# Optimization experiments

Hardware: AMD Instinct MI355X
Metric: run time of the kernel (lower is better)

Reference implementation:

```python
import jax, jax.numpy as jnp
import numpy as np

B, N, FIN, H, F = 8, 1024, 256, 8, 64
NEG_SLOPE = 0.2


def setup_inputs() -> dict:
    key = jax.random.key(0)
    k = jax.random.split(key, 6)
    x = jax.random.normal(k[0], (B, N, FIN), dtype=jnp.float32)
    adj_mask = jax.random.randint(k[1], (B, N, N), 0, 2, dtype=jnp.int32)
    edge_prior = jax.random.normal(k[2], (B, N, N), dtype=jnp.float32)
    # params (xavier-style scales)
    W = jax.random.normal(k[3], (FIN, H * F), dtype=jnp.float32) * np.sqrt(2.0 / (FIN + H * F))
    a_left = jax.random.normal(k[4], (H, F), dtype=jnp.float32) * np.sqrt(2.0 / (1 + F))
    a_right = jax.random.normal(k[5], (H, F), dtype=jnp.float32) * np.sqrt(2.0 / (1 + F))
    edge_scale = jnp.float32(0.05)
    return {"x": x, "adj_mask": adj_mask, "edge_prior": edge_prior,
            "W": W, "a_left": a_left, "a_right": a_right, "edge_scale": edge_scale}


def reference(x, adj_mask, edge_prior, W, a_left, a_right, edge_scale):
    b, n, _ = x.shape
    h = (x @ W).reshape(b, n, H, F)                      # [B,N,H,F]
    e_left = jnp.einsum('bnhf,hf->bnh', h, a_left)       # [B,N,H]
    e_right = jnp.einsum('bnhf,hf->bnh', h, a_right)     # [B,N,H]
    e = jax.nn.leaky_relu(e_left[:, :, None, :] + e_right[:, None, :, :],
                          negative_slope=NEG_SLOPE)      # [B,N,N,H]
    e = e + edge_scale * edge_prior[..., None]
    e = jnp.where((adj_mask == 0)[..., None], -jnp.inf, e)
    alpha = jax.nn.softmax(e, axis=2)                    # softmax over neighbors j
    h_new = jnp.einsum('bijh,bjhf->bihf', alpha, h)      # [B,N,H,F]
    return h_new.reshape(b, n, H * F)                    # concat=True
```

## Files before the change

kernel.cpp:

```cpp
#include <hip/hip_runtime.h>
#include <hip/hip_bf16.h>

#define B_ 8
#define N_ 1024
#define FIN_ 256
#define H_ 8
#define F_ 64
#define HF_ 512
#define BN_ 8192
#define LOG2E 1.4426950408889634f

using bf16x8 = __attribute__((ext_vector_type(8))) short;
using f32x4  = __attribute__((ext_vector_type(4))) float;
using i32x4  = __attribute__((ext_vector_type(4))) int;

__device__ __forceinline__ short f2bf(float x) {
  __hip_bfloat16 b = __float2bfloat16(x);
  return *reinterpret_cast<short*>(&b);
}
__device__ __forceinline__ float bf2f(short s) {
  union { unsigned u; float f; } v;
  v.u = ((unsigned)(unsigned short)s) << 16;
  return v.f;
}
__device__ __forceinline__ bf16x8 cvtCE(f32x4 pa, f32x4 pb, i32x4 ma, i32x4 mb, float es) {
  bf16x8 o;
#pragma unroll
  for (int e = 0; e < 4; e++) {
    o[e]     = f2bf(ma[e] != 0 ? es * pa[e] : -1e30f);
    o[e + 4] = f2bf(mb[e] != 0 ? es * pb[e] : -1e30f);
  }
  return o;
}

__global__ __launch_bounds__(256) void k_cvt(
    const float* __restrict__ x, const float* __restrict__ W,
    short* __restrict__ xb, short* __restrict__ Wt) {
  const int bid = blockIdx.x;
  if (bid < 1024) {
    const int idx = (bid * 256 + threadIdx.x) * 8;
    f32x4 a = *(const f32x4*)(x + idx);
    f32x4 b = *(const f32x4*)(x + idx + 4);
    bf16x8 o;
    o[0]=f2bf(a[0]); o[1]=f2bf(a[1]); o[2]=f2bf(a[2]); o[3]=f2bf(a[3]);
    o[4]=f2bf(b[0]); o[5]=f2bf(b[1]); o[6]=f2bf(b[2]); o[7]=f2bf(b[3]);
    *(bf16x8*)(xb + idx) = o;
  } else {
    const int idx = (bid - 1024) * 256 + threadIdx.x;
    const int f = idx >> 8, c = idx & 255;
    Wt[f * FIN_ + c] = f2bf(W[c * HF_ + f]);
  }
}

__global__ __launch_bounds__(256) void k_pre(
    const float* __restrict__ prior, const int* __restrict__ mask,
    const float* __restrict__ esp, short* __restrict__ cmat) {
  const int b  = blockIdx.x & 7;
  const int it = blockIdx.x >> 3;
  const int t  = threadIdx.x;
  const int i  = t >> 3;
  const int jb = (t & 7) * 8;
  const float es = esp[0] * LOG2E;
  const size_t rowbase = ((size_t)b * N_ + it * 32 + i) * N_;
  short* cmt = cmat + (size_t)(b * 32 + it) * 32768
             + (i >> 4) * 512 + (i & 15) * 8;
#pragma unroll
  for (int jt = 0; jt < 16; jt++) {
    const int j = jt * 64 + jb;
    f32x4 p0 = *(const f32x4*)(prior + rowbase + j);
    f32x4 p1 = *(const f32x4*)(prior + rowbase + j + 4);
    i32x4 m0 = *(const i32x4*)(mask + rowbase + j);
    i32x4 m1 = *(const i32x4*)(mask + rowbase + j + 4);
    *(bf16x8*)(cmt + (j >> 5) * 1024 + ((j >> 3) & 3) * 128) =
        cvtCE(p0, p1, m0, m1, es);
  }
}

__global__ __launch_bounds__(256) void k_h(
    const short* __restrict__ Wt, const short* __restrict__ xb,
    const float* __restrict__ aL, const float* __restrict__ aR,
    short* __restrict__ hAg, float* __restrict__ el_t, float* __restrict__ er_t) {
  const int nt = blockIdx.x;
  const int h  = blockIdx.y;
  const int w  = threadIdx.x >> 6;
  const int l  = threadIdx.x & 63;
  const int lr = l & 15, lk = l >> 4;
  const int n0 = nt * 64;
  const int fbase = h * 64 + w * 16;

  f32x4 acc[4] = {};
  const short* arow = Wt + (fbase + lr) * FIN_ + lk * 8;

#pragma unroll
  for (int k0 = 0; k0 < FIN_; k0 += 32) {
    bf16x8 a = *(const bf16x8*)(arow + k0);
#pragma unroll
    for (int nf = 0; nf < 4; nf++) {
      bf16x8 bb = *(const bf16x8*)(xb + (size_t)(n0 + nf * 16 + lr) * FIN_ + k0 + lk * 8);
      acc[nf] = __builtin_amdgcn_mfma_f32_16x16x32_bf16(a, bb, acc[nf], 0, 0, 0);
    }
  }

  __shared__ short sT[64][72];
  __shared__ float sEl[4][64], sEr[4][64];
  float al[4], ar[4];
#pragma unroll
  for (int r = 0; r < 4; r++) {
    const int fl = w * 16 + lk * 4 + r;
    al[r] = aL[h * F_ + fl];
    ar[r] = aR[h * F_ + fl];
  }
#pragma unroll
  for (int nf = 0; nf < 4; nf++) {
    const int nl = nf * 16 + lr;
#pragma unroll
    for (int r = 0; r < 4; r++)
      sT[w * 16 + lk * 4 + r][nl] = f2bf(acc[nf][r]);
    float pl = acc[nf][0]*al[0] + acc[nf][1]*al[1] + acc[nf][2]*al[2] + acc[nf][3]*al[3];
    float pr = acc[nf][0]*ar[0] + acc[nf][1]*ar[1] + acc[nf][2]*ar[2] + acc[nf][3]*ar[3];
    pl += __shfl_xor(pl, 16); pl += __shfl_xor(pl, 32);
    pr += __shfl_xor(pr, 16); pr += __shfl_xor(pr, 32);
    if (lk == 0) { sEl[w][nl] = pl; sEr[w][nl] = pr; }
  }
  __syncthreads();
  if (threadIdx.x < 64) {
    const int n = threadIdx.x;
    el_t[h * BN_ + n0 + n] = (sEl[0][n] + sEl[1][n] + sEl[2][n] + sEl[3][n]) * LOG2E;
    er_t[h * BN_ + n0 + n] = (sEr[0][n] + sEr[1][n] + sEr[2][n] + sEr[3][n]) * LOG2E;
  }
  const int b8h = (nt >> 4) * 8 + h;
  const int jb  = (nt & 15) * 2;
#pragma unroll
  for (int gi = 0; gi < 2; gi++) {
    const int g   = threadIdx.x * 2 + gi;
    const int jsl = g >> 8, ff = (g >> 6) & 3, gl = g & 63;
    const int glr = gl & 15, glk = gl >> 4;
    bf16x8 v = *(const bf16x8*)(&sT[ff * 16 + glr][jsl * 32 + glk * 8]);
    *(bf16x8*)(hAg + (((size_t)b8h * 32 + jb + jsl) * 4 + ff) * 512 + gl * 8) = v;
  }
}

#define PREFX(sn, Hd, E0d, E1d, Cd)                                   \
  {                                                                   \
    const short* hs_ = hW + (size_t)(sn) * 2048;                      \
    Hd[0] = *(const bf16x8*)(hs_);                                    \
    Hd[1] = *(const bf16x8*)(hs_ + 512);                              \
    Hd[2] = *(const bf16x8*)(hs_ + 1024);                             \
    Hd[3] = *(const bf16x8*)(hs_ + 1536);                             \
    E0d   = *(const f32x4*)(erp + (sn) * 32);                         \
    E1d   = *(const f32x4*)(erp + (sn) * 32 + 4);                     \
    Cd[0] = *(const bf16x8*)(cmW + (size_t)(sn) * 1024);              \
    Cd[1] = *(const bf16x8*)(cmW + (size_t)(sn) * 1024 + 512);        \
  }

#define COMP2(Hu, Cu, E0u, E1u)                                                \
  {                                                                            \
    bf16x8 pfA, pfB;                                                           \
    _Pragma("unroll")                                                          \
    for (int q = 0; q < 4; q++) {                                              \
      const float e0 = E0u[q], e1 = E1u[q];                                    \
      float sA  = el0 + e0, sA2 = el0 + e1;                                    \
      float sB  = el1 + e0, sB2 = el1 + e1;                                    \
      float vA  = fmaf(0.6f, sA,  bf2f(Cu[0][q]));                             \
      vA  = fmaf(0.4f, fabsf(sA),  vA);                                        \
      float vA2 = fmaf(0.6f, sA2, bf2f(Cu[0][q + 4]));                         \
      vA2 = fmaf(0.4f, fabsf(sA2), vA2);                                       \
      float vB  = fmaf(0.6f, sB,  bf2f(Cu[1][q]));                             \
      vB  = fmaf(0.4f, fabsf(sB),  vB);                                        \
      float vB2 = fmaf(0.6f, sB2, bf2f(Cu[1][q + 4]));                         \
      vB2 = fmaf(0.4f, fabsf(sB2), vB2);                                       \
      float x1_, x2_, x3_, x4_;                                                \
      asm("v_exp_f32 %0, %1" : "=v"(x1_) : "v"(vA));                           \
      asm("v_exp_f32 %0, %1" : "=v"(x2_) : "v"(vA2));                          \
      asm("v_exp_f32 %0, %1" : "=v"(x3_) : "v"(vB));                           \
      asm("v_exp_f32 %0, %1" : "=v"(x4_) : "v"(vB2));                          \
      pfA[q] = f2bf(x1_); pfA[q + 4] = f2bf(x2_);                              \
      pfB[q] = f2bf(x3_); pfB[q + 4] = f2bf(x4_);                              \
    }                                                                          \
    __builtin_amdgcn_s_setprio(1);                                             \
    accSA   = __builtin_amdgcn_mfma_f32_16x16x32_bf16(ones, pfA, accSA, 0,0,0);\
    accSB   = __builtin_amdgcn_mfma_f32_16x16x32_bf16(ones, pfB, accSB, 0,0,0);\
    accA[0] = __builtin_amdgcn_mfma_f32_16x16x32_bf16(Hu[0], pfA, accA[0],0,0,0);\
    accB[0] = __builtin_amdgcn_mfma_f32_16x16x32_bf16(Hu[0], pfB, accB[0],0,0,0);\
    accA[1] = __builtin_amdgcn_mfma_f32_16x16x32_bf16(Hu[1], pfA, accA[1],0,0,0);\
    accB[1] = __builtin_amdgcn_mfma_f32_16x16x32_bf16(Hu[1], pfB, accB[1],0,0,0);\
    accA[2] = __builtin_amdgcn_mfma_f32_16x16x32_bf16(Hu[2], pfA, accA[2],0,0,0);\
    accB[2] = __builtin_amdgcn_mfma_f32_16x16x32_bf16(Hu[2], pfB, accB[2],0,0,0);\
    accA[3] = __builtin_amdgcn_mfma_f32_16x16x32_bf16(Hu[3], pfA, accA[3],0,0,0);\
    accB[3] = __builtin_amdgcn_mfma_f32_16x16x32_bf16(Hu[3], pfB, accB[3],0,0,0);\
    __builtin_amdgcn_s_setprio(0);                                             \
  }

__global__ __launch_bounds__(256, 2) void k_attn(
    const short* __restrict__ hAg, const float* __restrict__ el_t,
    const float* __restrict__ er_t, const short* __restrict__ cmat,
    float* __restrict__ out) {
  const int bid = blockIdx.x;
  const int b  = bid & 7;
  const int hp = (bid >> 3) & 1;
  const int it = bid >> 4;
  const int t  = threadIdx.x;
  const int h  = hp * 4 + (t >> 6);
  const int l  = t & 63;
  const int lr = l & 15, lk = l >> 4;
  const int i0 = it * 32;
  const size_t bn = (size_t)b * N_;

  const float el0 = el_t[h * BN_ + bn + i0 + lr];
  const float el1 = el_t[h * BN_ + bn + i0 + 16 + lr];
  const float* erp = er_t + h * BN_ + bn + lk * 8;
  const short* hW  = hAg + (size_t)(b * 8 + h) * 65536 + l * 8;
  const short* cmW = cmat + (size_t)(b * 32 + it) * 32768 + l * 8;

  bf16x8 HA[4], HB[4], HC[4], HD[4];
  bf16x8 cA[2], cB[2], cC[2], cD[2];
  f32x4 eA0, eA1, eB0, eB1, eC0, eC1, eD0, eD1;
  f32x4 accA[4] = {}, accB[4] = {};
  f32x4 accSA = {}, accSB = {};
  bf16x8 ones;
#pragma unroll
  for (int e = 0; e < 8; e++) ones[e] = (short)0x3F80;

  PREFX(0, HA, eA0, eA1, cA);
  PREFX(1, HB, eB0, eB1, cB);
  PREFX(2, HC, eC0, eC1, cC);
  PREFX(3, HD, eD0, eD1, cD);

  for (int s = 0; s < 32; s += 4) {
    COMP2(HA, cA, eA0, eA1);  PREFX(s + 4, HA, eA0, eA1, cA);
    COMP2(HB, cB, eB0, eB1);  PREFX(s + 5, HB, eB0, eB1, cB);
    COMP2(HC, cC, eC0, eC1);  PREFX(s + 6, HC, eC0, eC1, cC);
    COMP2(HD, cD, eD0, eD1);  PREFX(s + 7, HD, eD0, eD1, cD);
  }

  const float invA = 1.0f / accSA[0];
  const float invB = 1.0f / accSB[0];
  const size_t rowA = bn + i0 + lr;
  const size_t rowB = rowA + 16;
#pragma unroll
  for (int ff = 0; ff < 4; ff++) {
    f32x4 va = accA[ff], vb = accB[ff];
    va[0]*=invA; va[1]*=invA; va[2]*=invA; va[3]*=invA;
    vb[0]*=invB; vb[1]*=invB; vb[2]*=invB; vb[3]*=invB;
    *(f32x4*)(out + rowA * HF_ + h * 64 + ff * 16 + lk * 4) = va;
    *(f32x4*)(out + rowB * HF_ + h * 64 + ff * 16 + lk * 4) = vb;
  }
}

extern "C" void kernel_launch(void* const* d_in, const int* in_sizes, int n_in,
                              void* d_out, int out_size, void* d_ws, size_t ws_size,
                              hipStream_t stream) {
  const float* x     = (const float*)d_in[0];
  const int*   adj   = (const int*)  d_in[1];
  const float* prior = (const float*)d_in[2];
  const float* W     = (const float*)d_in[3];
  const float* aL    = (const float*)d_in[4];
  const float* aR    = (const float*)d_in[5];
  const float* es    = (const float*)d_in[6];
  float* out = (float*)d_out;

  char* ws = (char*)d_ws;
  short* hAg  = (short*)ws;
  short* xb   = (short*)(ws + 8u  * 1024 * 1024);
  short* Wt   = (short*)(ws + 12u * 1024 * 1024);
  float* el_t = (float*)(ws + 12u * 1024 * 1024 + 262144);
  float* er_t = (float*)(ws + 12u * 1024 * 1024 + 524288);
  short* cmat = (short*)(ws + 13u * 1024 * 1024);

  hipLaunchKernelGGL(k_cvt, dim3(1536), dim3(256), 0, stream, x, W, xb, Wt);
  hipLaunchKernelGGL(k_pre, dim3(256), dim3(256), 0, stream, prior, adj, es, cmat);
  hipLaunchKernelGGL(k_h,   dim3(128, 8), dim3(256), 0, stream,
                     Wt, xb, aL, aR, hAg, el_t, er_t);
  hipLaunchKernelGGL(k_attn, dim3(512), dim3(256), 0, stream,
                     hAg, el_t, er_t, cmat, out);
}
```

Before: 67.29 us.

## Merge conversion and prior/mask prep kernels, stage cmat through swizzled LDS

Combines the x/W bf16 conversion kernel and the prior/mask preprocessing kernel into one launch with a block-index split, removing a kernel launch and letting both kinds of work run concurrently. The prior/mask blocks now write their bf16 tile into a 64KB shared buffer with an XOR swizzle and then copy it out to global memory with fully contiguous 16-byte stores. Previously those global stores were scattered. The large shared allocation applies to every block, including the conversion blocks that never use it, which limits occupancy.

```diff
diff --git a/kernel.cpp b/kernel.cpp
--- a/kernel.cpp
+++ b/kernel.cpp
@@ -33,37 +33,38 @@
   return o;
 }
 
-__global__ __launch_bounds__(256) void k_cvt(
+__global__ __launch_bounds__(256) void k_prep(
     const float* __restrict__ x, const float* __restrict__ W,
-    short* __restrict__ xb, short* __restrict__ Wt) {
+    const float* __restrict__ prior, const int* __restrict__ mask,
+    const float* __restrict__ esp,
+    short* __restrict__ xb, short* __restrict__ Wt, short* __restrict__ cmat) {
   const int bid = blockIdx.x;
-  if (bid < 1024) {
-    const int idx = (bid * 256 + threadIdx.x) * 8;
-    f32x4 a = *(const f32x4*)(x + idx);
-    f32x4 b = *(const f32x4*)(x + idx + 4);
-    bf16x8 o;
-    o[0]=f2bf(a[0]); o[1]=f2bf(a[1]); o[2]=f2bf(a[2]); o[3]=f2bf(a[3]);
-    o[4]=f2bf(b[0]); o[5]=f2bf(b[1]); o[6]=f2bf(b[2]); o[7]=f2bf(b[3]);
-    *(bf16x8*)(xb + idx) = o;
-  } else {
-    const int idx = (bid - 1024) * 256 + threadIdx.x;
-    const int f = idx >> 8, c = idx & 255;
-    Wt[f * FIN_ + c] = f2bf(W[c * HF_ + f]);
-  }
-}
-
-__global__ __launch_bounds__(256) void k_pre(
-    const float* __restrict__ prior, const int* __restrict__ mask,
-    const float* __restrict__ esp, short* __restrict__ cmat) {
-  const int b  = blockIdx.x & 7;
-  const int it = blockIdx.x >> 3;
-  const int t  = threadIdx.x;
-  const int i  = t >> 3;
+  const int t   = threadIdx.x;
+  if (bid >= 256) {
+    const int cid = bid - 256;
+    if (cid < 1024) {
+      const int idx = (cid * 256 + t) * 8;
+      f32x4 a = *(const f32x4*)(x + idx);
+      f32x4 b = *(const f32x4*)(x + idx + 4);
+      bf16x8 o;
+      o[0]=f2bf(a[0]); o[1]=f2bf(a[1]); o[2]=f2bf(a[2]); o[3]=f2bf(a[3]);
+      o[4]=f2bf(b[0]); o[5]=f2bf(b[1]); o[6]=f2bf(b[2]); o[7]=f2bf(b[3]);
+      *(bf16x8*)(xb + idx) = o;
+    } else {
+      const int idx = (cid - 1024) * 256 + t;
+      const int f = idx >> 8, c = idx & 255;
+      Wt[f * FIN_ + c] = f2bf(W[c * HF_ + f]);
+    }
+    return;
+  }
+  __shared__ short stile[32768];
+  const int b  = bid & 7;
+  const int it = bid >> 3;
+  const float es = esp[0] * LOG2E;
+  const int r  = t >> 3;
   const int jb = (t & 7) * 8;
-  const float es = esp[0] * LOG2E;
-  const size_t rowbase = ((size_t)b * N_ + it * 32 + i) * N_;
-  short* cmt = cmat + (size_t)(b * 32 + it) * 32768
-             + (i >> 4) * 512 + (i & 15) * 8;
+  const int frag = r >> 4, rl = r & 15;
+  const size_t rowbase = ((size_t)b * N_ + it * 32 + r) * (size_t)N_;
 #pragma unroll
   for (int jt = 0; jt < 16; jt++) {
     const int j = jt * 64 + jb;
@@ -71,8 +72,23 @@
     f32x4 p1 = *(const f32x4*)(prior + rowbase + j + 4);
     i32x4 m0 = *(const i32x4*)(mask + rowbase + j);
     i32x4 m1 = *(const i32x4*)(mask + rowbase + j + 4);
-    *(bf16x8*)(cmt + (j >> 5) * 1024 + ((j >> 3) & 3) * 128) =
-        cvtCE(p0, p1, m0, m1, es);
+    const int s = j >> 5;
+    const int l = ((j >> 3) & 3) * 16 + rl;
+    const int lsw = l ^ (2 * (l >> 4)) ^ ((s & 1) << 3);
+    *(bf16x8*)(&stile[s * 1024 + frag * 512 + lsw * 8]) = cvtCE(p0, p1, m0, m1, es);
+  }
+  __syncthreads();
+  short* cmt = cmat + (size_t)(b * 32 + it) * 32768;
+#pragma unroll
+  for (int k = 0; k < 16; k++) {
+    const int g   = k * 2048 + t * 8;
+    const int s   = g >> 10;
+    const int rem = g & 1023;
+    const int fr  = rem >> 9;
+    const int l   = (rem >> 3) & 63;
+    const int lsw = l ^ (2 * (l >> 4)) ^ ((s & 1) << 3);
+    bf16x8 v = *(const bf16x8*)(&stile[s * 1024 + fr * 512 + lsw * 8]);
+    *(bf16x8*)(cmt + g) = v;
   }
 }
 
@@ -267,8 +283,8 @@
   float* er_t = (float*)(ws + 12u * 1024 * 1024 + 524288);
   short* cmat = (short*)(ws + 13u * 1024 * 1024);
 
-  hipLaunchKernelGGL(k_cvt, dim3(1536), dim3(256), 0, stream, x, W, xb, Wt);
-  hipLaunchKernelGGL(k_pre, dim3(256), dim3(256), 0, stream, prior, adj, es, cmat);
+  hipLaunchKernelGGL(k_prep, dim3(1792), dim3(256), 0, stream,
+                     x, W, prior, adj, es, xb, Wt, cmat);
   hipLaunchKernelGGL(k_h,   dim3(128, 8), dim3(256), 0, stream,
                      Wt, xb, aL, aR, hAg, el_t, er_t);
   hipLaunchKernelGGL(k_attn, dim3(512), dim3(256), 0, stream,
```

Measured after the change: 64.55 us. 1.04x faster.
